# Kernel tuning notes

Hardware: AMD Instinct MI355X
Metric: run time of the kernel (lower is better)

The kernel has to match this reference:

```python
import jax, jax.numpy as jnp
import numpy as np

N_NODES = 50000


def _gcn_conv(x, W, b, row, col, n):
    # GCNConv (PyG defaults): h = x @ W; add self-loops; symmetric deg normalization; scatter-add; + bias
    h = x @ W
    loops = jnp.arange(n, dtype=row.dtype)
    r = jnp.concatenate([row, loops])
    c = jnp.concatenate([col, loops])
    deg = jax.ops.segment_sum(jnp.ones(r.shape[0], dtype=h.dtype), c, num_segments=n)
    dinv = jnp.where(deg > 0, jax.lax.rsqrt(deg), 0.0)
    norm = dinv[r] * dinv[c]  # [E+n]
    msgs = h[r] * norm[:, None]  # gather + scale
    out = jax.ops.segment_sum(msgs, c, num_segments=n)  # scatter-add to targets
    return out + b


def setup_inputs() -> dict:
    key = jax.random.key(0)
    k1, k2, k3, k4 = jax.random.split(key, 4)
    f_in, hid, f_out = 256, 512, 250
    n, e = N_NODES, 1600000
    x = jax.random.normal(k1, (n, f_in), dtype=jnp.float32)
    edge_index = jax.random.randint(k2, (2, e), 0, n, dtype=jnp.int32)
    W1 = jax.random.normal(k3, (f_in, hid), dtype=jnp.float32) * (1.0 / np.sqrt(f_in))
    b1 = jnp.zeros((hid,), dtype=jnp.float32)
    W2 = jax.random.normal(k4, (hid, f_out), dtype=jnp.float32) * (1.0 / np.sqrt(hid))
    b2 = jnp.zeros((f_out,), dtype=jnp.float32)
    return {"x": x, "edge_index": edge_index, "W1": W1, "b1": b1, "W2": W2, "b2": b2}


def reference(x, edge_index, W1, b1, W2, b2):
    row, col = edge_index[0], edge_index[1]
    n = x.shape[0]
    h = jax.nn.relu(_gcn_conv(x, W1, b1, row, col, n))
    out = jax.nn.relu(_gcn_conv(h, W2, b2, row, col, n))
    return out
```

## Files before the change

### kernel.cpp

```cpp
#include <hip/hip_runtime.h>
#include <hip/hip_bf16.h>


#define F_IN  256
#define F_HID 512
#define F_OUT 250

using bf16x8 = __attribute__((ext_vector_type(8))) short;
using f32x4  = __attribute__((ext_vector_type(4))) float;

__device__ __forceinline__ ushort f32_bf16_rne(float f) {
    uint u = __float_as_uint(f);
    u += 0x7FFFu + ((u >> 16) & 1u);
    return (ushort)(u >> 16);
}
__device__ __forceinline__ float bf16u_f32(ushort h) {
    return __uint_as_float(((uint)h) << 16);
}


__global__ __launch_bounds__(256) void init_kernel(int* cnt, int* cursor, int n) {
    int i = blockIdx.x * 256 + threadIdx.x;
    if (i < n) { cnt[i] = 0; cursor[i] = 0; }
}

__global__ __launch_bounds__(256) void hist_kernel(const int* __restrict__ col, int* cnt, int E) {
    int e = blockIdx.x * 256 + threadIdx.x;
    if (e < E) atomicAdd(&cnt[col[e]], 1);
}

__global__ __launch_bounds__(256) void dinv_kernel(const int* __restrict__ cnt, float* dinv, int n) {
    int i = blockIdx.x * 256 + threadIdx.x;
    if (i < n) dinv[i] = rsqrtf((float)(cnt[i] + 1));
}

__global__ __launch_bounds__(1024) void scan_kernel(const int* __restrict__ cnt, int* rowptr, int n) {
    __shared__ int wsum[16];
    __shared__ int carry_s;
    int t = threadIdx.x;
    int wid = t >> 6, lane = t & 63;
    if (t == 0) carry_s = 0;
    __syncthreads();
    for (int base = 0; base < n; base += 1024) {
        int i = base + t;
        int v = (i < n) ? cnt[i] : 0;
        int s = v;
        #pragma unroll
        for (int off = 1; off < 64; off <<= 1) {
            int u = __shfl_up(s, off, 64);
            if (lane >= off) s += u;
        }
        if (lane == 63) wsum[wid] = s;
        __syncthreads();
        if (wid == 0 && lane < 16) {
            int ws = wsum[lane];
            #pragma unroll
            for (int off = 1; off < 16; off <<= 1) {
                int u = __shfl_up(ws, off, 64);
                if (lane >= off) ws += u;
            }
            wsum[lane] = ws;
        }
        __syncthreads();
        int wbase = (wid == 0) ? 0 : wsum[wid - 1];
        int carry = carry_s;
        if (i < n) rowptr[i] = carry + wbase + s - v;
        __syncthreads();
        if (t == 1023) carry_s = carry + wbase + s;
        __syncthreads();
    }
    if (t == 0) rowptr[n] = carry_s;
}

__global__ __launch_bounds__(256) void fill_kernel(const int* __restrict__ row, const int* __restrict__ col,
                                                   const int* __restrict__ rowptr, int* cursor,
                                                   int* csr, int E) {
    int e = blockIdx.x * 256 + threadIdx.x;
    if (e < E) {
        int c = col[e];
        int p = rowptr[c] + atomicAdd(&cursor[c], 1);
        csr[p] = row[e];
    }
}


__global__ __launch_bounds__(256) void wsplit_kernel(const float* __restrict__ W,
                                                     ushort* __restrict__ WThi, ushort* __restrict__ WTlo,
                                                     int K, int N) {
    __shared__ float tile[32][33];
    int t = threadIdx.x;
    int k0 = blockIdx.x * 32, n0 = blockIdx.y * 32;
    int r = t >> 3, c = (t & 7) * 4;
    #pragma unroll
    for (int q = 0; q < 4; ++q) {
        float z = 0.f;
        if (n0 + c + q < N) z = W[(size_t)(k0 + r) * N + n0 + c + q];
        tile[r][c + q] = z;
    }
    __syncthreads();
    int nr = t >> 3, kq = (t & 7) * 4;
    int gn = n0 + nr;
    if (gn < N) {
        ushort4 h4, l4;
        ushort* hp = &h4.x; ushort* lp = &l4.x;
        #pragma unroll
        for (int q = 0; q < 4; ++q) {
            float z = tile[kq + q][nr];
            ushort h = f32_bf16_rne(z);
            hp[q] = h;
            lp[q] = f32_bf16_rne(z - bf16u_f32(h));
        }
        *(ushort4*)&WThi[(size_t)gn * K + k0 + kq] = h4;
        *(ushort4*)&WTlo[(size_t)gn * K + k0 + kq] = l4;
    }
}


template<int F, int LDX, bool BIAS_RELU, bool SPLIT_OUT>
__global__ __launch_bounds__(256) void agg_kernel(const float* __restrict__ X,
                                                  const float* __restrict__ dinv,
                                                  const int* __restrict__ rowptr,
                                                  const int* __restrict__ csr,
                                                  const float* __restrict__ bias,
                                                  float* __restrict__ out,
                                                  ushort* __restrict__ outHi, ushort* __restrict__ outLo,
                                                  int ldo, int n) {
    int c = blockIdx.x * 4 + (threadIdx.x >> 6);
    if (c >= n) return;
    int l = threadIdx.x & 63;
    int f0 = l * 4;
    float dc = dinv[c];

    float4 acc;
    {
        float4 v = *(const float4*)(X + (size_t)c * LDX + f0);
        acc.x = v.x * dc; acc.y = v.y * dc; acc.z = v.z * dc; acc.w = v.w * dc;
    }
    int beg = rowptr[c], end = rowptr[c + 1];
    #pragma unroll 4
    for (int j = beg; j < end; ++j) {
        int r = csr[j];
        float dr = dinv[r];
        float4 v = *(const float4*)(X + (size_t)r * LDX + f0);
        acc.x += dr * v.x; acc.y += dr * v.y; acc.z += dr * v.z; acc.w += dr * v.w;
    }
    acc.x *= dc; acc.y *= dc; acc.z *= dc; acc.w *= dc;

    if (SPLIT_OUT) {
        ushort4 h4, l4;
        float a4[4] = {acc.x, acc.y, acc.z, acc.w};
        ushort* hp = &h4.x; ushort* lp = &l4.x;
        #pragma unroll
        for (int q = 0; q < 4; ++q) {
            ushort h = f32_bf16_rne(a4[q]);
            hp[q] = h;
            lp[q] = f32_bf16_rne(a4[q] - bf16u_f32(h));
        }
        *(ushort4*)(outHi + (size_t)c * F + f0) = h4;
        *(ushort4*)(outLo + (size_t)c * F + f0) = l4;
        return;
    }

    float* op = out + (size_t)c * ldo + f0;
    if (BIAS_RELU) {
        float b[4];
        #pragma unroll
        for (int q = 0; q < 4; ++q) b[q] = (f0 + q < F) ? bias[f0 + q] : 0.f;
        acc.x = fmaxf(acc.x + b[0], 0.f);
        acc.y = fmaxf(acc.y + b[1], 0.f);
        acc.z = fmaxf(acc.z + b[2], 0.f);
        acc.w = fmaxf(acc.w + b[3], 0.f);
        if (f0 + 3 < F) {
            ((float2*)op)[0] = make_float2(acc.x, acc.y);
            ((float2*)op)[1] = make_float2(acc.z, acc.w);
        } else {
            float a4[4] = {acc.x, acc.y, acc.z, acc.w};
            #pragma unroll
            for (int q = 0; q < 4; ++q)
                if (f0 + q < F) op[q] = a4[q];
        }
    } else {
        *(float4*)op = acc;
    }
}


template<bool SPLIT_OUT>
__global__ __launch_bounds__(256) void gemm_mfma(const ushort* __restrict__ Ahi, const ushort* __restrict__ Alo,
                                                 const ushort* __restrict__ Bhi, const ushort* __restrict__ Blo,
                                                 const float* __restrict__ bias,
                                                 float* __restrict__ Cf,
                                                 ushort* __restrict__ Chi, ushort* __restrict__ Clo,
                                                 int M, int N, int K, int ldc) {
    __shared__ ushort As_hi[128][40];
    __shared__ ushort As_lo[128][40];
    __shared__ ushort Bs_hi[128][40];
    __shared__ ushort Bs_lo[128][40];

    int t = threadIdx.x;
    int row0 = blockIdx.x * 128;
    int col0 = blockIdx.y * 128;
    int lane = t & 63;
    int w = t >> 6;
    int wr = w >> 1, wc = w & 1;
    int lr = lane & 15, lg = lane >> 4;

    int srow = t >> 2;
    int soct = (t & 3) * 8;

    f32x4 acc[4][4];
    #pragma unroll
    for (int i = 0; i < 4; ++i)
        #pragma unroll
        for (int j = 0; j < 4; ++j)
            acc[i][j] = (f32x4){0.f, 0.f, 0.f, 0.f};

    for (int k0 = 0; k0 < K; k0 += 32) {
        #pragma unroll
        for (int h = 0; h < 2; ++h) {
            int r = srow + h * 64;
            int4 zero = make_int4(0, 0, 0, 0);
            int ga = row0 + r;
            int4 vh = zero, vl = zero;
            if (ga < M) {
                vh = *(const int4*)(Ahi + (size_t)ga * K + k0 + soct);
                vl = *(const int4*)(Alo + (size_t)ga * K + k0 + soct);
            }
            *(int4*)&As_hi[r][soct] = vh;
            *(int4*)&As_lo[r][soct] = vl;
            int gb = col0 + r;
            int4 wh = zero, wl = zero;
            if (gb < N) {
                wh = *(const int4*)(Bhi + (size_t)gb * K + k0 + soct);
                wl = *(const int4*)(Blo + (size_t)gb * K + k0 + soct);
            }
            *(int4*)&Bs_hi[r][soct] = wh;
            *(int4*)&Bs_lo[r][soct] = wl;
        }
        __syncthreads();

        bf16x8 ah[4], al[4], bh[4], bl[4];
        #pragma unroll
        for (int mi = 0; mi < 4; ++mi) {
            ah[mi] = *(const bf16x8*)&As_hi[wr * 64 + mi * 16 + lr][lg * 8];
            al[mi] = *(const bf16x8*)&As_lo[wr * 64 + mi * 16 + lr][lg * 8];
        }
        #pragma unroll
        for (int ni = 0; ni < 4; ++ni) {
            bh[ni] = *(const bf16x8*)&Bs_hi[wc * 64 + ni * 16 + lr][lg * 8];
            bl[ni] = *(const bf16x8*)&Bs_lo[wc * 64 + ni * 16 + lr][lg * 8];
        }
        #pragma unroll
        for (int mi = 0; mi < 4; ++mi)
            #pragma unroll
            for (int ni = 0; ni < 4; ++ni) {
                acc[mi][ni] = __builtin_amdgcn_mfma_f32_16x16x32_bf16(ah[mi], bh[ni], acc[mi][ni], 0, 0, 0);
                acc[mi][ni] = __builtin_amdgcn_mfma_f32_16x16x32_bf16(ah[mi], bl[ni], acc[mi][ni], 0, 0, 0);
                acc[mi][ni] = __builtin_amdgcn_mfma_f32_16x16x32_bf16(al[mi], bh[ni], acc[mi][ni], 0, 0, 0);
            }
        __syncthreads();
    }

    #pragma unroll
    for (int mi = 0; mi < 4; ++mi) {
        int rbase = row0 + wr * 64 + mi * 16 + lg * 4;
        #pragma unroll
        for (int ni = 0; ni < 4; ++ni) {
            int cg = col0 + wc * 64 + ni * 16 + lr;
            f32x4 a = acc[mi][ni];
            if (SPLIT_OUT) {
                float bia = bias[cg];
                #pragma unroll
                for (int r = 0; r < 4; ++r) {
                    int rg = rbase + r;
                    if (rg < M) {
                        float z = fmaxf(a[r] + bia, 0.f);
                        ushort h = f32_bf16_rne(z);
                        Chi[(size_t)rg * N + cg] = h;
                        Clo[(size_t)rg * N + cg] = f32_bf16_rne(z - bf16u_f32(h));
                    }
                }
            } else {
                if (cg < N) {
                    #pragma unroll
                    for (int r = 0; r < 4; ++r) {
                        int rg = rbase + r;
                        if (rg < M) Cf[(size_t)rg * ldc + cg] = a[r];
                    }
                }
            }
        }
    }
}


extern "C" void kernel_launch(void* const* d_in, const int* in_sizes, int n_in,
                              void* d_out, int out_size, void* d_ws, size_t ws_size,
                              hipStream_t stream) {
    const float* x   = (const float*)d_in[0];
    const int*   ei  = (const int*)d_in[1];
    const float* W1  = (const float*)d_in[2];
    const float* b1  = (const float*)d_in[3];
    const float* W2  = (const float*)d_in[4];
    const float* b2  = (const float*)d_in[5];
    float* out = (float*)d_out;

    const int n = in_sizes[0] / F_IN;
    const int E = in_sizes[1] / 2;
    const int* row = ei;
    const int* col = ei + E;

    char* p = (char*)d_ws;
    auto alloc = [&](size_t bytes) { void* r = (void*)p; p += (bytes + 255) & ~(size_t)255; return r; };
    int*    cnt    = (int*)alloc((size_t)n * 4);
    int*    cursor = (int*)alloc((size_t)n * 4);
    int*    rowptr = (int*)alloc((size_t)(n + 1) * 4);
    int*    csr    = (int*)alloc((size_t)E * 4);
    float*  dinv   = (float*)alloc((size_t)n * 4);
    ushort* Ahi    = (ushort*)alloc((size_t)n * F_IN * 2);
    ushort* Alo    = (ushort*)alloc((size_t)n * F_IN * 2);
    ushort* Hhi    = (ushort*)alloc((size_t)n * F_HID * 2);
    ushort* Hlo    = (ushort*)alloc((size_t)n * F_HID * 2);
    ushort* W1Thi  = (ushort*)alloc((size_t)F_HID * F_IN * 2);
    ushort* W1Tlo  = (ushort*)alloc((size_t)F_HID * F_IN * 2);
    ushort* W2Thi  = (ushort*)alloc((size_t)F_OUT * F_HID * 2);
    ushort* W2Tlo  = (ushort*)alloc((size_t)F_OUT * F_HID * 2);
    float*  bufY   = (float*)Ahi;

    int nb_n = (n + 255) / 256;
    int nb_e = (E + 255) / 256;

    init_kernel<<<nb_n, 256, 0, stream>>>(cnt, cursor, n);
    hist_kernel<<<nb_e, 256, 0, stream>>>(col, cnt, E);
    dinv_kernel<<<nb_n, 256, 0, stream>>>(cnt, dinv, n);
    scan_kernel<<<1, 1024, 0, stream>>>(cnt, rowptr, n);
    fill_kernel<<<nb_e, 256, 0, stream>>>(row, col, rowptr, cursor, csr, E);

    {
        dim3 g1(F_IN / 32, F_HID / 32);
        wsplit_kernel<<<g1, 256, 0, stream>>>(W1, W1Thi, W1Tlo, F_IN, F_HID);
        dim3 g2(F_HID / 32, (F_OUT + 31) / 32);
        wsplit_kernel<<<g2, 256, 0, stream>>>(W2, W2Thi, W2Tlo, F_HID, F_OUT);
    }

    int nb_agg = (n + 3) / 4;

    agg_kernel<F_IN, F_IN, false, true><<<nb_agg, 256, 0, stream>>>(
        x, dinv, rowptr, csr, nullptr, nullptr, Ahi, Alo, F_IN, n);
    {
        dim3 grid((n + 127) / 128, F_HID / 128);
        gemm_mfma<true><<<grid, 256, 0, stream>>>(Ahi, Alo, W1Thi, W1Tlo, b1,
                                                  nullptr, Hhi, Hlo, n, F_HID, F_IN, F_HID);
    }
    {
        dim3 grid((n + 127) / 128, (F_OUT + 127) / 128);
        gemm_mfma<false><<<grid, 256, 0, stream>>>(Hhi, Hlo, W2Thi, W2Tlo, nullptr,
                                                   bufY, nullptr, nullptr, n, F_OUT, F_HID, 256);
    }
    agg_kernel<F_OUT, 256, true, false><<<nb_agg, 256, 0, stream>>>(
        bufY, dinv, rowptr, csr, b2, out, nullptr, nullptr, F_OUT, n);
}
```

Baseline: 904.6 us.

## Pack source degree into CSR entries, prescale GEMM output, batch gathers by eight

The fill step now stores each source index together with its dinv value in an int2 CSR, so aggregation no longer does a dependent random load of dinv per edge. The second GEMM multiplies its output rows by dinv, which lets the second aggregation skip per-edge scaling. The edge loop is unrolled by eight with all index and feature loads issued before accumulation, to raise memory-level parallelism. The init kernel is replaced by a memset. In exchange, CSR memory traffic doubles and register pressure in the aggregation kernel goes up.

```diff
diff --git a/kernel.cpp b/kernel.cpp
--- a/kernel.cpp
+++ b/kernel.cpp
@@ -18,11 +18,6 @@
     return __uint_as_float(((uint)h) << 16);
 }
 
-
-__global__ __launch_bounds__(256) void init_kernel(int* cnt, int* cursor, int n) {
-    int i = blockIdx.x * 256 + threadIdx.x;
-    if (i < n) { cnt[i] = 0; cursor[i] = 0; }
-}
 
 __global__ __launch_bounds__(256) void hist_kernel(const int* __restrict__ col, int* cnt, int E) {
     int e = blockIdx.x * 256 + threadIdx.x;
@@ -74,12 +69,14 @@
 
 __global__ __launch_bounds__(256) void fill_kernel(const int* __restrict__ row, const int* __restrict__ col,
                                                    const int* __restrict__ rowptr, int* cursor,
-                                                   int* csr, int E) {
+                                                   const float* __restrict__ dinv,
+                                                   int2* __restrict__ csrd, int E) {
     int e = blockIdx.x * 256 + threadIdx.x;
     if (e < E) {
         int c = col[e];
+        int r = row[e];
         int p = rowptr[c] + atomicAdd(&cursor[c], 1);
-        csr[p] = row[e];
+        csrd[p] = make_int2(r, __float_as_int(dinv[r]));
     }
 }
 
@@ -116,11 +113,11 @@
 }
 
 
-template<int F, int LDX, bool BIAS_RELU, bool SPLIT_OUT>
+template<int F, int LDX, bool BIAS_RELU, bool SPLIT_OUT, bool PRESCALED>
 __global__ __launch_bounds__(256) void agg_kernel(const float* __restrict__ X,
                                                   const float* __restrict__ dinv,
                                                   const int* __restrict__ rowptr,
-                                                  const int* __restrict__ csr,
+                                                  const int2* __restrict__ csrd,
                                                   const float* __restrict__ bias,
                                                   float* __restrict__ out,
                                                   ushort* __restrict__ outHi, ushort* __restrict__ outLo,
@@ -134,15 +131,40 @@
     float4 acc;
     {
         float4 v = *(const float4*)(X + (size_t)c * LDX + f0);
-        acc.x = v.x * dc; acc.y = v.y * dc; acc.z = v.z * dc; acc.w = v.w * dc;
-    }
+        if (PRESCALED) { acc = v; }
+        else { acc.x = v.x * dc; acc.y = v.y * dc; acc.z = v.z * dc; acc.w = v.w * dc; }
+    }
+
     int beg = rowptr[c], end = rowptr[c + 1];
-    #pragma unroll 4
-    for (int j = beg; j < end; ++j) {
-        int r = csr[j];
-        float dr = dinv[r];
-        float4 v = *(const float4*)(X + (size_t)r * LDX + f0);
-        acc.x += dr * v.x; acc.y += dr * v.y; acc.z += dr * v.z; acc.w += dr * v.w;
+    int j = beg;
+    for (; j + 8 <= end; j += 8) {
+        int2 e8[8];
+        #pragma unroll
+        for (int q = 0; q < 8; ++q) e8[q] = csrd[j + q];
+        float4 v[8];
+        #pragma unroll
+        for (int q = 0; q < 8; ++q)
+            v[q] = *(const float4*)(X + (size_t)e8[q].x * LDX + f0);
+        #pragma unroll
+        for (int q = 0; q < 8; ++q) {
+            if (PRESCALED) {
+                acc.x += v[q].x; acc.y += v[q].y; acc.z += v[q].z; acc.w += v[q].w;
+            } else {
+                float dr = __int_as_float(e8[q].y);
+                acc.x += dr * v[q].x; acc.y += dr * v[q].y;
+                acc.z += dr * v[q].z; acc.w += dr * v[q].w;
+            }
+        }
+    }
+    for (; j < end; ++j) {
+        int2 e = csrd[j];
+        float4 v = *(const float4*)(X + (size_t)e.x * LDX + f0);
+        if (PRESCALED) {
+            acc.x += v.x; acc.y += v.y; acc.z += v.z; acc.w += v.w;
+        } else {
+            float dr = __int_as_float(e.y);
+            acc.x += dr * v.x; acc.y += dr * v.y; acc.z += dr * v.z; acc.w += dr * v.w;
+        }
     }
     acc.x *= dc; acc.y *= dc; acc.z *= dc; acc.w *= dc;
 
@@ -189,6 +211,7 @@
 __global__ __launch_bounds__(256) void gemm_mfma(const ushort* __restrict__ Ahi, const ushort* __restrict__ Alo,
                                                  const ushort* __restrict__ Bhi, const ushort* __restrict__ Blo,
                                                  const float* __restrict__ bias,
+                                                 const float* __restrict__ dinv,
                                                  float* __restrict__ Cf,
                                                  ushort* __restrict__ Chi, ushort* __restrict__ Clo,
                                                  int M, int N, int K, int ldc) {
@@ -285,7 +308,7 @@
                     #pragma unroll
                     for (int r = 0; r < 4; ++r) {
                         int rg = rbase + r;
-                        if (rg < M) Cf[(size_t)rg * ldc + cg] = a[r];
+                        if (rg < M) Cf[(size_t)rg * ldc + cg] = a[r] * dinv[rg];
                     }
                 }
             }
@@ -315,8 +338,8 @@
     int*    cnt    = (int*)alloc((size_t)n * 4);
     int*    cursor = (int*)alloc((size_t)n * 4);
     int*    rowptr = (int*)alloc((size_t)(n + 1) * 4);
-    int*    csr    = (int*)alloc((size_t)E * 4);
     float*  dinv   = (float*)alloc((size_t)n * 4);
+    int2*   csrd   = (int2*)alloc((size_t)E * 8);
     ushort* Ahi    = (ushort*)alloc((size_t)n * F_IN * 2);
     ushort* Alo    = (ushort*)alloc((size_t)n * F_IN * 2);
     ushort* Hhi    = (ushort*)alloc((size_t)n * F_HID * 2);
@@ -330,11 +353,11 @@
     int nb_n = (n + 255) / 256;
     int nb_e = (E + 255) / 256;
 
-    init_kernel<<<nb_n, 256, 0, stream>>>(cnt, cursor, n);
+    hipMemsetAsync(cnt, 0, (char*)rowptr - (char*)cnt, stream);
     hist_kernel<<<nb_e, 256, 0, stream>>>(col, cnt, E);
     dinv_kernel<<<nb_n, 256, 0, stream>>>(cnt, dinv, n);
     scan_kernel<<<1, 1024, 0, stream>>>(cnt, rowptr, n);
-    fill_kernel<<<nb_e, 256, 0, stream>>>(row, col, rowptr, cursor, csr, E);
+    fill_kernel<<<nb_e, 256, 0, stream>>>(row, col, rowptr, cursor, dinv, csrd, E);
 
     {
         dim3 g1(F_IN / 32, F_HID / 32);
@@ -345,18 +368,18 @@
 
     int nb_agg = (n + 3) / 4;
 
-    agg_kernel<F_IN, F_IN, false, true><<<nb_agg, 256, 0, stream>>>(
-        x, dinv, rowptr, csr, nullptr, nullptr, Ahi, Alo, F_IN, n);
+    agg_kernel<F_IN, F_IN, false, true, false><<<nb_agg, 256, 0, stream>>>(
+        x, dinv, rowptr, csrd, nullptr, nullptr, Ahi, Alo, F_IN, n);
     {
         dim3 grid((n + 127) / 128, F_HID / 128);
-        gemm_mfma<true><<<grid, 256, 0, stream>>>(Ahi, Alo, W1Thi, W1Tlo, b1,
+        gemm_mfma<true><<<grid, 256, 0, stream>>>(Ahi, Alo, W1Thi, W1Tlo, b1, nullptr,
                                                   nullptr, Hhi, Hlo, n, F_HID, F_IN, F_HID);
     }
     {
         dim3 grid((n + 127) / 128, (F_OUT + 127) / 128);
-        gemm_mfma<false><<<grid, 256, 0, stream>>>(Hhi, Hlo, W2Thi, W2Tlo, nullptr,
+        gemm_mfma<false><<<grid, 256, 0, stream>>>(Hhi, Hlo, W2Thi, W2Tlo, nullptr, dinv,
                                                    bufY, nullptr, nullptr, n, F_OUT, F_HID, 256);
     }
-    agg_kernel<F_OUT, 256, true, false><<<nb_agg, 256, 0, stream>>>(
-        bufY, dinv, rowptr, csr, b2, out, nullptr, nullptr, F_OUT, n);
-}
+    agg_kernel<F_OUT, 256, true, false, true><<<nb_agg, 256, 0, stream>>>(
+        bufY, dinv, rowptr, csrd, b2, out, nullptr, nullptr, F_OUT, n);
+}
```

Result: no change. 917.0 us (+1.4%).
